# Optimization experiments

Hardware: AMD Instinct MI355X
Metric: run time of the kernel (lower is better)

## Reference

```python
import jax, jax.numpy as jnp
import numpy as np

D_MODEL = 512
NUM_HEADS = 8
D_K = D_MODEL // NUM_HEADS  # 64
LN_EPS = 1e-5


def setup_inputs() -> dict:
    key = jax.random.key(0)
    ks = jax.random.split(key, 6)
    B, S, D = 8, 1024, D_MODEL
    scale = 1.0 / np.sqrt(D)
    return {
        "query": jax.random.normal(ks[0], (B, S, D), jnp.float32),
        "key": jax.random.normal(ks[1], (B, S, D), jnp.float32),
        "value": jax.random.normal(ks[2], (B, S, D), jnp.float32),
        "Wq": jax.random.normal(ks[3], (D, D), jnp.float32) * scale,
        "bq": jnp.zeros((D,), jnp.float32),
        "Wk": jax.random.normal(ks[4], (D, D), jnp.float32) * scale,
        "bk": jnp.zeros((D,), jnp.float32),
        "Wo": jax.random.normal(ks[5], (D, D * NUM_HEADS), jnp.float32) * (1.0 / np.sqrt(D * NUM_HEADS)),
        "bo": jnp.zeros((D,), jnp.float32),
        "gamma": jnp.ones((D,), jnp.float32),
        "beta": jnp.zeros((D,), jnp.float32),
    }


def reference(query, key, value, Wq, bq, Wk, bk, Wo, bo, gamma, beta):
    B, S, D = value.shape
    h, dk = NUM_HEADS, D_K
    # QK projections -> [B, h, S, dk]
    q = (query @ Wq.T + bq).reshape(B, S, h, dk).transpose(0, 2, 1, 3)
    k = (key @ Wk.T + bk).reshape(B, S, h, dk).transpose(0, 2, 1, 3)
    # scaled dot-product scores [B, h, Sq, Sk]
    scores = jnp.einsum("bhqd,bhkd->bhqk", q, k) / jnp.sqrt(jnp.asarray(dk, q.dtype))
    attn = jax.nn.softmax(scores, axis=-1)
    # value broadcast across heads: value is [B, Sk, D] -> per-head output [B, h, Sq, D]
    x = jnp.einsum("bhqk,bkd->bhqd", attn, value)
    # concat heads -> [B, Sq, h*D], output projection back to D
    x = x.transpose(0, 2, 1, 3).reshape(B, S, h * D)
    x = x @ Wo.T + bo
    # residual + LayerNorm (dropout = identity in eval)
    y = value + x
    mu = jnp.mean(y, axis=-1, keepdims=True)
    var = jnp.var(y, axis=-1, keepdims=True)
    out = (y - mu) * jax.lax.rsqrt(var + LN_EPS) * gamma + beta
    return out, attn
```

## Files before the change

### kernel.cpp

```cpp
#include <hip/hip_runtime.h>
#include <hip/hip_bf16.h>

#define B_ 8
#define S_ 1024
#define D_ 512
#define H_ 8
#define DK_ 64
#define HD_ 4096

typedef __attribute__((ext_vector_type(8))) short bf16x8;
typedef __attribute__((ext_vector_type(4))) float f32x4;

static __device__ __forceinline__ unsigned short f2bf(float f) {
    unsigned u = __float_as_uint(f);
    unsigned r = (u + 0x7fffu + ((u >> 16) & 1u)) >> 16;
    return (unsigned short)r;
}

static __device__ __forceinline__ void gload16(const unsigned short* g, unsigned short* l) {
    __builtin_amdgcn_global_load_lds(
        (const __attribute__((address_space(1))) void*)g,
        (__attribute__((address_space(3))) void*)l, 16, 0, 0);
}

static __device__ __forceinline__ int plidx(int ql, int k) {
    return ql * 1024 + ((((k >> 3) ^ (ql & 7))) << 3) + (k & 7);
}

__global__ __launch_bounds__(256) void prep_kernel(
    const float* __restrict__ query, unsigned short* __restrict__ Xq,
    const float* __restrict__ key,   unsigned short* __restrict__ Xk,
    const float* __restrict__ Wq,    unsigned short* __restrict__ Wqbf,
    const float* __restrict__ Wk,    unsigned short* __restrict__ Wkbf,
    const float* __restrict__ Wo,    unsigned short* __restrict__ Wobf,
    const float* __restrict__ V,     unsigned short* __restrict__ Vt)
{
    __shared__ float tile[32][33];
    const int bid = blockIdx.x;
    const int t = threadIdx.x;
    if (bid < 10752) {
        const float* s; unsigned short* d; int lb;
        if      (bid < 4096) { s = query; d = Xq;   lb = bid; }
        else if (bid < 8192) { s = key;   d = Xk;   lb = bid - 4096; }
        else if (bid < 8448) { s = Wq;    d = Wqbf; lb = bid - 8192; }
        else if (bid < 8704) { s = Wk;    d = Wkbf; lb = bid - 8448; }
        else                 { s = Wo;    d = Wobf; lb = bid - 8704; }
        const size_t i = ((size_t)lb * 256 + t) * 4;
        float4 v = *(const float4*)&s[i];
        ushort4 u = { f2bf(v.x), f2bf(v.y), f2bf(v.z), f2bf(v.w) };
        *(ushort4*)&d[i] = u;
    } else {
        const int idx = bid - 10752;
        const int s0 = (idx & 31) * 32;
        const int e0 = ((idx >> 5) & 15) * 32;
        const int b  = idx >> 9;
        const int r = t >> 3, c4 = (t & 7) * 4;
        float4 v = *(const float4*)&V[((size_t)b * S_ + s0 + r) * D_ + e0 + c4];
        tile[r][c4 + 0] = v.x; tile[r][c4 + 1] = v.y;
        tile[r][c4 + 2] = v.z; tile[r][c4 + 3] = v.w;
        __syncthreads();
        ushort4 u;
        u.x = f2bf(tile[c4 + 0][r]); u.y = f2bf(tile[c4 + 1][r]);
        u.z = f2bf(tile[c4 + 2][r]); u.w = f2bf(tile[c4 + 3][r]);
        *(ushort4*)&Vt[((size_t)b * D_ + e0 + r) * S_ + s0 + c4] = u;
    }
}

template<int KDIM, int TN, int MODE>
static __device__ __forceinline__ void gemm_body(
    const unsigned short* __restrict__ A, const unsigned short* __restrict__ Bw,
    const float* __restrict__ bias, const float* __restrict__ Vres,
    void* __restrict__ Out, float scale, int nb)
{
    constexpr int NB = 512 / TN;
    constexpr int CF = TN / 32;
    const int m0 = (nb / NB) * 128;
    const int n0 = (nb % NB) * TN;

    __shared__ __align__(16) unsigned short As[2][128 * 32];
    __shared__ __align__(16) unsigned short Bs[2][TN * 32];

    const int t = threadIdx.x;
    const int wave = t >> 6, lane = t & 63;
    const int wr = wave >> 1, wc = wave & 1;
    const int lr = lane & 15, g = lane >> 4;
    const int gx = (g ^ (lr & 3)) << 3;

    f32x4 acc[4][CF];
    #pragma unroll
    for (int r = 0; r < 4; ++r)
        #pragma unroll
        for (int c = 0; c < CF; ++c) acc[r][c] = (f32x4){0.f, 0.f, 0.f, 0.f};

    const int sub = lane >> 2;
    const int cb  = (((lane & 3) ^ (sub & 3)) << 3);

    auto stage = [&](int buf, int k0) {
        #pragma unroll
        for (int s = 0; s < 2; ++s) {
            const int chunk = s * 4 + wave;
            const int row = chunk * 16 + sub;
            if constexpr (MODE == 0) {
                gload16(&A[(size_t)(m0 + row) * KDIM + k0 + cb], &As[buf][chunk * 512]);
            } else {
                const int m = m0 + row;
                const int bb = m >> 10, ss = m & 1023;
                const int h = k0 >> 9;
                gload16(&A[(((size_t)(bb * H_ + h)) * S_ + ss) * D_ + (k0 & 511) + cb],
                        &As[buf][chunk * 512]);
            }
        }
        #pragma unroll
        for (int s = 0; s < TN / 64; ++s) {
            const int chunk = s * 4 + wave;
            const int row = chunk * 16 + sub;
            gload16(&Bw[(size_t)(n0 + row) * KDIM + k0 + cb], &Bs[buf][chunk * 512]);
        }
    };
    auto compute = [&](int cur) {
        bf16x8 af[4], bfr[CF];
        #pragma unroll
        for (int r = 0; r < 4; ++r)
            af[r] = *(const bf16x8*)&As[cur][(wr * 64 + r * 16 + lr) * 32 + gx];
        #pragma unroll
        for (int c = 0; c < CF; ++c)
            bfr[c] = *(const bf16x8*)&Bs[cur][(wc * (TN / 2) + c * 16 + lr) * 32 + gx];
        __builtin_amdgcn_s_setprio(1);
        #pragma unroll
        for (int c = 0; c < CF; ++c)
            #pragma unroll
            for (int r = 0; r < 4; ++r)
                acc[r][c] = __builtin_amdgcn_mfma_f32_16x16x32_bf16(af[r], bfr[c], acc[r][c], 0, 0, 0);
        __builtin_amdgcn_s_setprio(0);
    };

    const int NT = KDIM / 32;
    stage(0, 0);
    __syncthreads();
    int cur = 0;
    for (int tt = 0; tt < NT - 1; ++tt) {
        stage(cur ^ 1, (tt + 1) * 32);
        compute(cur);
        __syncthreads();
        cur ^= 1;
    }
    compute(cur);

    float bn[CF];
    #pragma unroll
    for (int c = 0; c < CF; ++c) bn[c] = bias[n0 + wc * (TN / 2) + c * 16 + lr];

    #pragma unroll
    for (int r = 0; r < 4; ++r) {
        #pragma unroll
        for (int c = 0; c < CF; ++c) {
            const int n = n0 + wc * (TN / 2) + c * 16 + lr;
            #pragma unroll
            for (int i = 0; i < 4; ++i) {
                const int m = m0 + wr * 64 + r * 16 + g * 4 + i;
                if constexpr (MODE == 0) {
                    const int srow = m & 1023, bb = m >> 10;
                    const int h = n >> 6, dk = n & 63;
                    ((unsigned short*)Out)[(((size_t)(bb * H_ + h)) * S_ + srow) * DK_ + dk] =
                        f2bf((acc[r][c][i] + bn[c]) * scale);
                } else {
                    const size_t oo = (size_t)m * D_ + n;
                    ((float*)Out)[oo] = acc[r][c][i] + bn[c] + Vres[oo];
                }
            }
        }
    }
}

__global__ __launch_bounds__(256) void proj2_kernel(
    const unsigned short* __restrict__ Xq, const unsigned short* __restrict__ Wqbf,
    const float* __restrict__ bq, unsigned short* __restrict__ Qbf,
    const unsigned short* __restrict__ Xk, const unsigned short* __restrict__ Wkbf,
    const float* __restrict__ bk, unsigned short* __restrict__ Kbf)
{
    const int o = blockIdx.x;
    const bool isQ = o < 512;
    const int ol = isQ ? o : o - 512;
    const int nb = (ol % 8) * 64 + ol / 8;
    gemm_body<512, 64, 0>(isQ ? Xq : Xk, isQ ? Wqbf : Wkbf,
                          isQ ? bq : bk, nullptr,
                          (void*)(isQ ? Qbf : Kbf), isQ ? 0.125f : 1.0f, nb);
}

__global__ __launch_bounds__(256) void out_gemm(
    const unsigned short* __restrict__ AV, const unsigned short* __restrict__ Wobf,
    const float* __restrict__ bo, const float* __restrict__ Vres,
    float* __restrict__ Y)
{
    const int o = blockIdx.x;
    const int nb = (o % 8) * 64 + o / 8;
    gemm_body<4096, 64, 1>(AV, Wobf, bo, Vres, (void*)Y, 0.f, nb);
}

__global__ __launch_bounds__(1024, 4) void fused_attn(
    const unsigned short* __restrict__ Qbf,
    const unsigned short* __restrict__ Kbf,
    const unsigned short* __restrict__ Vt,
    float* __restrict__ attn,
    unsigned short* __restrict__ AV)
{
    const int o = blockIdx.x;
    const int nb = (o & 7) * 128 + (o >> 3);
    const int bh = nb >> 4;
    const int q0 = (nb & 15) * 64;
    const int b = bh >> 3;
    const unsigned short* Qb = Qbf + (size_t)bh * S_ * DK_;
    const unsigned short* Kb = Kbf + (size_t)bh * S_ * DK_;
    const unsigned short* Vb = Vt + (size_t)b * D_ * S_;
    float* outp = attn + ((size_t)bh << 20);

    __shared__ unsigned short PL[64 * 1024];
    __shared__ float redm[64][16];
    __shared__ float rowm[64];

    const int t = threadIdx.x;
    const int wave = t >> 6, lane = t & 63;
    const int wcol = wave * 64;
    const int lr = lane & 15;
    const int g  = lane >> 4;

    f32x4 acc[4][4];
    #pragma unroll
    for (int r = 0; r < 4; ++r)
        #pragma unroll
        for (int c = 0; c < 4; ++c) acc[r][c] = (f32x4){0.f, 0.f, 0.f, 0.f};

    #pragma unroll
    for (int kk = 0; kk < 2; ++kk) {
        bf16x8 af[4];
        #pragma unroll
        for (int r = 0; r < 4; ++r)
            af[r] = *(const bf16x8*)&Kb[(size_t)(wcol + r * 16 + lr) * DK_ + kk * 32 + g * 8];
        bf16x8 qf[4];
        #pragma unroll
        for (int c = 0; c < 4; ++c)
            qf[c] = *(const bf16x8*)&Qb[(size_t)(q0 + c * 16 + lr) * DK_ + kk * 32 + g * 8];
        __builtin_amdgcn_s_setprio(1);
        #pragma unroll
        for (int r = 0; r < 4; ++r)
            #pragma unroll
            for (int c = 0; c < 4; ++c)
                acc[r][c] = __builtin_amdgcn_mfma_f32_16x16x32_bf16(af[r], qf[c], acc[r][c], 0, 0, 0);
        __builtin_amdgcn_s_setprio(0);
    }

    float sloc[4];
    #pragma unroll
    for (int c = 0; c < 4; ++c) {
        float s = 0.f;
        #pragma unroll
        for (int r = 0; r < 4; ++r)
            #pragma unroll
            for (int i = 0; i < 4; ++i) {
                float p = __expf(acc[r][c][i]);
                acc[r][c][i] = p;
                s += p;
            }
        s += __shfl_xor(s, 16);
        s += __shfl_xor(s, 32);
        sloc[c] = s;
    }
    if (lane < 16) {
        #pragma unroll
        for (int c = 0; c < 4; ++c) redm[c * 16 + lane][wave] = sloc[c];
    }
    __syncthreads();
    if (t < 64) {
        float s = redm[t][0];
        #pragma unroll
        for (int w = 1; w < 16; ++w) s += redm[t][w];
        rowm[t] = 1.0f / s;
    }
    __syncthreads();

    #pragma unroll
    for (int c = 0; c < 4; ++c) {
        const int ql = c * 16 + lr;
        const float ri = rowm[ql];
        #pragma unroll
        for (int r = 0; r < 4; ++r) {
            f32x4 v = acc[r][c];
            v[0] *= ri; v[1] *= ri; v[2] *= ri; v[3] *= ri;
            const int k = wcol + r * 16 + g * 4;
            unsigned p01, p23;
            asm("v_cvt_pk_bf16_f32 %0, %1, %2" : "=v"(p01) : "v"(v[0]), "v"(v[1]));
            asm("v_cvt_pk_bf16_f32 %0, %1, %2" : "=v"(p23) : "v"(v[2]), "v"(v[3]));
            uint2 pk = { p01, p23 };
            *(uint2*)&PL[plidx(ql, k)] = pk;
        }
    }
    __syncthreads();

    if (wave >= 8) {
        #pragma unroll
        for (int jj = 0; jj < 8; ++jj) {
            const int row = (wave - 8) * 8 + jj;
            const int ps = lane ^ (row & 7);
            float* rowp = outp + ((size_t)(q0 + row) << 10);
            uint4 u0 = *(const uint4*)&PL[row * 1024 + (ps << 3)];
            uint4 u1 = *(const uint4*)&PL[row * 1024 + ((64 + ps) << 3)];
            f32x4 f0, f1, f2, f3;
            f0[0] = __uint_as_float((u0.x & 0xffffu) << 16);
            f0[1] = __uint_as_float(u0.x & 0xffff0000u);
            f0[2] = __uint_as_float((u0.y & 0xffffu) << 16);
            f0[3] = __uint_as_float(u0.y & 0xffff0000u);
            f1[0] = __uint_as_float((u0.z & 0xffffu) << 16);
            f1[1] = __uint_as_float(u0.z & 0xffff0000u);
            f1[2] = __uint_as_float((u0.w & 0xffffu) << 16);
            f1[3] = __uint_as_float(u0.w & 0xffff0000u);
            f2[0] = __uint_as_float((u1.x & 0xffffu) << 16);
            f2[1] = __uint_as_float(u1.x & 0xffff0000u);
            f2[2] = __uint_as_float((u1.y & 0xffffu) << 16);
            f2[3] = __uint_as_float(u1.y & 0xffff0000u);
            f3[0] = __uint_as_float((u1.z & 0xffffu) << 16);
            f3[1] = __uint_as_float(u1.z & 0xffff0000u);
            f3[2] = __uint_as_float((u1.w & 0xffffu) << 16);
            f3[3] = __uint_as_float(u1.w & 0xffff0000u);
            const int k0f = lane * 8;
            *(f32x4*)&rowp[k0f]           = f0;
            *(f32x4*)&rowp[k0f + 4]       = f1;
            *(f32x4*)&rowp[512 + k0f]     = f2;
            *(f32x4*)&rowp[512 + k0f + 4] = f3;
        }
    } else {
        const int we = wave * 64;
        f32x4 accv[4][4];
        #pragma unroll
        for (int r = 0; r < 4; ++r)
            #pragma unroll
            for (int c = 0; c < 4; ++c) accv[r][c] = (f32x4){0.f, 0.f, 0.f, 0.f};

        bf16x8 vf[4];
        #pragma unroll
        for (int c = 0; c < 4; ++c)
            vf[c] = *(const bf16x8*)&Vb[(size_t)(we + c * 16 + lr) * S_ + g * 8];

        for (int k0 = 0; k0 < S_; k0 += 32) {
            const int kn = k0 + 32;
            bf16x8 nvf[4];
            if (kn < S_) {
                #pragma unroll
                for (int c = 0; c < 4; ++c)
                    nvf[c] = *(const bf16x8*)&Vb[(size_t)(we + c * 16 + lr) * S_ + kn + g * 8];
            }
            bf16x8 pa[4];
            #pragma unroll
            for (int r = 0; r < 4; ++r)
                pa[r] = *(const bf16x8*)&PL[plidx(r * 16 + lr, k0 + g * 8)];
            __builtin_amdgcn_s_setprio(1);
            #pragma unroll
            for (int c = 0; c < 4; ++c)
                #pragma unroll
                for (int r = 0; r < 4; ++r)
                    accv[r][c] = __builtin_amdgcn_mfma_f32_16x16x32_bf16(pa[r], vf[c], accv[r][c], 0, 0, 0);
            __builtin_amdgcn_s_setprio(0);
            if (kn < S_) {
                #pragma unroll
                for (int c = 0; c < 4; ++c) vf[c] = nvf[c];
            }
        }

        #pragma unroll
        for (int r = 0; r < 4; ++r) {
            #pragma unroll
            for (int c = 0; c < 4; ++c) {
                const int e = we + c * 16 + lr;
                #pragma unroll
                for (int i = 0; i < 4; ++i) {
                    const int row = q0 + r * 16 + g * 4 + i;
                    AV[((size_t)bh * S_ + row) * D_ + e] = f2bf(accv[r][c][i]);
                }
            }
        }
    }
}

__global__ __launch_bounds__(256) void ln_kernel(
    float* __restrict__ Y, const float* __restrict__ gamma,
    const float* __restrict__ beta)
{
    const int lane = threadIdx.x & 63;
    const int wave = threadIdx.x >> 6;
    const size_t row = (size_t)blockIdx.x * 4 + wave;
    float* p = Y + row * D_;
    float4 v0 = *(float4*)&p[lane * 4];
    float4 v1 = *(float4*)&p[256 + lane * 4];
    float s = v0.x + v0.y + v0.z + v0.w + v1.x + v1.y + v1.z + v1.w;
    float q = v0.x * v0.x + v0.y * v0.y + v0.z * v0.z + v0.w * v0.w +
              v1.x * v1.x + v1.y * v1.y + v1.z * v1.z + v1.w * v1.w;
    #pragma unroll
    for (int m = 1; m < 64; m <<= 1) {
        s += __shfl_xor(s, m);
        q += __shfl_xor(q, m);
    }
    const float mu  = s * (1.f / 512.f);
    const float var = q * (1.f / 512.f) - mu * mu;
    const float r = rsqrtf(var + 1e-5f);
    const float4 g0 = *(const float4*)&gamma[lane * 4];
    const float4 g1 = *(const float4*)&gamma[256 + lane * 4];
    const float4 b0 = *(const float4*)&beta[lane * 4];
    const float4 b1 = *(const float4*)&beta[256 + lane * 4];
    v0.x = (v0.x - mu) * r * g0.x + b0.x;
    v0.y = (v0.y - mu) * r * g0.y + b0.y;
    v0.z = (v0.z - mu) * r * g0.z + b0.z;
    v0.w = (v0.w - mu) * r * g0.w + b0.w;
    v1.x = (v1.x - mu) * r * g1.x + b1.x;
    v1.y = (v1.y - mu) * r * g1.y + b1.y;
    v1.z = (v1.z - mu) * r * g1.z + b1.z;
    v1.w = (v1.w - mu) * r * g1.w + b1.w;
    *(float4*)&p[lane * 4] = v0;
    *(float4*)&p[256 + lane * 4] = v1;
}

extern "C" void kernel_launch(void* const* d_in, const int* in_sizes, int n_in,
                              void* d_out, int out_size, void* d_ws, size_t ws_size,
                              hipStream_t stream)
{
    const float* query = (const float*)d_in[0];
    const float* key   = (const float*)d_in[1];
    const float* value = (const float*)d_in[2];
    const float* Wq    = (const float*)d_in[3];
    const float* bq    = (const float*)d_in[4];
    const float* Wk    = (const float*)d_in[5];
    const float* bk    = (const float*)d_in[6];
    const float* Wo    = (const float*)d_in[7];
    const float* bo    = (const float*)d_in[8];
    const float* gamma = (const float*)d_in[9];
    const float* beta  = (const float*)d_in[10];

    float* out  = (float*)d_out;
    float* attn = out + (size_t)B_ * S_ * D_;
    char*  attnB = (char*)attn;

    char* ws = (char*)d_ws;
    unsigned short* AV   = (unsigned short*)ws;
    unsigned short* Vt   = (unsigned short*)(ws + ((size_t)64 << 20));
    unsigned short* Wobf = (unsigned short*)(ws + ((size_t)72 << 20));
    unsigned short* Qbf  = (unsigned short*)d_out;
    unsigned short* Kbf  = (unsigned short*)d_out + ((size_t)4 << 20);
    unsigned short* Xq   = (unsigned short*)(attnB + ((size_t)200 << 20));
    unsigned short* Xk   = (unsigned short*)(attnB + ((size_t)210 << 20));
    unsigned short* Wqbf = (unsigned short*)(attnB + ((size_t)220 << 20));
    unsigned short* Wkbf = (unsigned short*)(attnB + ((size_t)221 << 20));

    prep_kernel<<<14848, 256, 0, stream>>>(query, Xq, key, Xk, Wq, Wqbf,
                                           Wk, Wkbf, Wo, Wobf, value, Vt);
    proj2_kernel<<<1024, 256, 0, stream>>>(Xq, Wqbf, bq, Qbf, Xk, Wkbf, bk, Kbf);
    fused_attn<<<1024, 1024, 0, stream>>>(Qbf, Kbf, Vt, attn, AV);
    out_gemm<<<512, 256, 0, stream>>>(AV, Wobf, bo, value, out);
    ln_kernel<<<2048, 256, 0, stream>>>(out, gamma, beta);
}
```

Before: 333.9 us.

## Write attention probabilities from registers and spread PV across all waves

The normalized softmax probabilities are now stored to the fp32 attention output straight from the MFMA accumulators, with no longer a second group of waves reading them back from LDS. With that role gone, all 16 waves take part in the P·V product, each covering 32 value columns instead of 64. This is meant to balance the work between the output-write path and the MFMA path, and to drop an LDS read plus bf16-to-fp32 unpack. The trade-off is a less contiguous global store pattern for the attention matrix, with 16-byte stores spread across rows. The attention output is also no longer bf16-rounded.

```diff
diff --git a/kernel.cpp b/kernel.cpp
--- a/kernel.cpp
+++ b/kernel.cpp
@@ -282,11 +282,13 @@
     for (int c = 0; c < 4; ++c) {
         const int ql = c * 16 + lr;
         const float ri = rowm[ql];
+        float* rowp = outp + ((size_t)(q0 + ql) << 10);
         #pragma unroll
         for (int r = 0; r < 4; ++r) {
             f32x4 v = acc[r][c];
             v[0] *= ri; v[1] *= ri; v[2] *= ri; v[3] *= ri;
             const int k = wcol + r * 16 + g * 4;
+            *(f32x4*)&rowp[k] = v;
             unsigned p01, p23;
             asm("v_cvt_pk_bf16_f32 %0, %1, %2" : "=v"(p01) : "v"(v[0]), "v"(v[1]));
             asm("v_cvt_pk_bf16_f32 %0, %1, %2" : "=v"(p23) : "v"(v[2]), "v"(v[3]));
@@ -296,85 +298,49 @@
     }
     __syncthreads();
 
-    if (wave >= 8) {
-        #pragma unroll
-        for (int jj = 0; jj < 8; ++jj) {
-            const int row = (wave - 8) * 8 + jj;
-            const int ps = lane ^ (row & 7);
-            float* rowp = outp + ((size_t)(q0 + row) << 10);
-            uint4 u0 = *(const uint4*)&PL[row * 1024 + (ps << 3)];
-            uint4 u1 = *(const uint4*)&PL[row * 1024 + ((64 + ps) << 3)];
-            f32x4 f0, f1, f2, f3;
-            f0[0] = __uint_as_float((u0.x & 0xffffu) << 16);
-            f0[1] = __uint_as_float(u0.x & 0xffff0000u);
-            f0[2] = __uint_as_float((u0.y & 0xffffu) << 16);
-            f0[3] = __uint_as_float(u0.y & 0xffff0000u);
-            f1[0] = __uint_as_float((u0.z & 0xffffu) << 16);
-            f1[1] = __uint_as_float(u0.z & 0xffff0000u);
-            f1[2] = __uint_as_float((u0.w & 0xffffu) << 16);
-            f1[3] = __uint_as_float(u0.w & 0xffff0000u);
-            f2[0] = __uint_as_float((u1.x & 0xffffu) << 16);
-            f2[1] = __uint_as_float(u1.x & 0xffff0000u);
-            f2[2] = __uint_as_float((u1.y & 0xffffu) << 16);
-            f2[3] = __uint_as_float(u1.y & 0xffff0000u);
-            f3[0] = __uint_as_float((u1.z & 0xffffu) << 16);
-            f3[1] = __uint_as_float(u1.z & 0xffff0000u);
-            f3[2] = __uint_as_float((u1.w & 0xffffu) << 16);
-            f3[3] = __uint_as_float(u1.w & 0xffff0000u);
-            const int k0f = lane * 8;
-            *(f32x4*)&rowp[k0f]           = f0;
-            *(f32x4*)&rowp[k0f + 4]       = f1;
-            *(f32x4*)&rowp[512 + k0f]     = f2;
-            *(f32x4*)&rowp[512 + k0f + 4] = f3;
-        }
-    } else {
-        const int we = wave * 64;
-        f32x4 accv[4][4];
-        #pragma unroll
-        for (int r = 0; r < 4; ++r)
+    const int we = wave * 32;
+    f32x4 accv[4][2];
+    #pragma unroll
+    for (int r = 0; r < 4; ++r)
+        #pragma unroll
+        for (int c = 0; c < 2; ++c) accv[r][c] = (f32x4){0.f, 0.f, 0.f, 0.f};
+
+    const unsigned short* vp0 = Vb + (size_t)(we + lr) * S_ + g * 8;
+    const unsigned short* vp1 = Vb + (size_t)(we + 16 + lr) * S_ + g * 8;
+    bf16x8 vf0 = *(const bf16x8*)vp0;
+    bf16x8 vf1 = *(const bf16x8*)vp1;
+
+    for (int k0 = 0; k0 < S_; k0 += 32) {
+        const int kn = k0 + 32;
+        bf16x8 nv0, nv1;
+        if (kn < S_) {
+            nv0 = *(const bf16x8*)(vp0 + kn);
+            nv1 = *(const bf16x8*)(vp1 + kn);
+        }
+        bf16x8 pa[4];
+        #pragma unroll
+        for (int r = 0; r < 4; ++r)
+            pa[r] = *(const bf16x8*)&PL[plidx(r * 16 + lr, k0 + g * 8)];
+        __builtin_amdgcn_s_setprio(1);
+        #pragma unroll
+        for (int r = 0; r < 4; ++r)
+            accv[r][0] = __builtin_amdgcn_mfma_f32_16x16x32_bf16(pa[r], vf0, accv[r][0], 0, 0, 0);
+        #pragma unroll
+        for (int r = 0; r < 4; ++r)
+            accv[r][1] = __builtin_amdgcn_mfma_f32_16x16x32_bf16(pa[r], vf1, accv[r][1], 0, 0, 0);
+        __builtin_amdgcn_s_setprio(0);
+        if (kn < S_) { vf0 = nv0; vf1 = nv1; }
+    }
+
+    #pragma unroll
+    for (int r = 0; r < 4; ++r) {
+        #pragma unroll
+        for (int c = 0; c < 2; ++c) {
+            const int e = we + c * 16 + lr;
             #pragma unroll
-            for (int c = 0; c < 4; ++c) accv[r][c] = (f32x4){0.f, 0.f, 0.f, 0.f};
-
-        bf16x8 vf[4];
-        #pragma unroll
-        for (int c = 0; c < 4; ++c)
-            vf[c] = *(const bf16x8*)&Vb[(size_t)(we + c * 16 + lr) * S_ + g * 8];
-
-        for (int k0 = 0; k0 < S_; k0 += 32) {
-            const int kn = k0 + 32;
-            bf16x8 nvf[4];
-            if (kn < S_) {
-                #pragma unroll
-                for (int c = 0; c < 4; ++c)
-                    nvf[c] = *(const bf16x8*)&Vb[(size_t)(we + c * 16 + lr) * S_ + kn + g * 8];
-            }
-            bf16x8 pa[4];
-            #pragma unroll
-            for (int r = 0; r < 4; ++r)
-                pa[r] = *(const bf16x8*)&PL[plidx(r * 16 + lr, k0 + g * 8)];
-            __builtin_amdgcn_s_setprio(1);
-            #pragma unroll
-            for (int c = 0; c < 4; ++c)
-                #pragma unroll
-                for (int r = 0; r < 4; ++r)
-                    accv[r][c] = __builtin_amdgcn_mfma_f32_16x16x32_bf16(pa[r], vf[c], accv[r][c], 0, 0, 0);
-            __builtin_amdgcn_s_setprio(0);
-            if (kn < S_) {
-                #pragma unroll
-                for (int c = 0; c < 4; ++c) vf[c] = nvf[c];
-            }
-        }
-
-        #pragma unroll
-        for (int r = 0; r < 4; ++r) {
-            #pragma unroll
-            for (int c = 0; c < 4; ++c) {
-                const int e = we + c * 16 + lr;
-                #pragma unroll
-                for (int i = 0; i < 4; ++i) {
-                    const int row = q0 + r * 16 + g * 4 + i;
-                    AV[((size_t)bh * S_ + row) * D_ + e] = f2bf(accv[r][c][i]);
-                }
+            for (int i = 0; i < 4; ++i) {
+                const int row = q0 + r * 16 + g * 4 + i;
+                AV[((size_t)bh * S_ + row) * D_ + e] = f2bf(accv[r][c][i]);
             }
         }
     }
```

New measurement: 334.0 us. No clear change (+0.0%).
